# Performance work log

Measured on AMD Instinct MI355X. Metric: run time of the kernel, lower is better.

Reference implementation:

```python
import jax, jax.numpy as jnp
import numpy as np

B, S, H = 2, 2048, 2048
NH, NKV, HD = 16, 4, 128
GROUPS = NH // NKV
THETA = 10000.0
EPS = 1e-6


def setup_inputs() -> dict:
    key = jax.random.key(0)
    ks = jax.random.split(key, 6)
    scale = 0.02
    return {
        "hidden_states": jax.random.normal(ks[0], (B, S, H), jnp.float32),
        "wq": jax.random.normal(ks[1], (NH * HD, H), jnp.float32) * scale,
        "wk": jax.random.normal(ks[2], (NKV * HD, H), jnp.float32) * scale,
        "wv": jax.random.normal(ks[3], (NKV * HD, H), jnp.float32) * scale,
        "wo": jax.random.normal(ks[4], (H, NH * HD), jnp.float32) * scale,
        "q_norm_weight": jnp.ones((HD,), jnp.float32),
        "k_norm_weight": jnp.ones((HD,), jnp.float32),
    }


def _rope_tables(seq_len):
    inv_freq = 1.0 / (THETA ** (jnp.arange(0, HD, 2, dtype=jnp.float32) / HD))
    t = jnp.arange(seq_len, dtype=jnp.float32)
    freqs = jnp.outer(t, inv_freq)              # [S, HD/2]
    emb = jnp.concatenate([freqs, freqs], -1)   # [S, HD]
    return jnp.cos(emb), jnp.sin(emb)


def _rotate_half(x):
    x1, x2 = x[..., : HD // 2], x[..., HD // 2:]
    return jnp.concatenate([-x2, x1], -1)


def _rmsnorm(x, w):
    var = jnp.mean(jnp.square(x), axis=-1, keepdims=True)
    return x * jax.lax.rsqrt(var + EPS) * w


def reference(hidden_states, wq, wk, wv, wo, q_norm_weight, k_norm_weight):
    b, s, _ = hidden_states.shape
    q = (hidden_states @ wq.T).reshape(b, s, NH, HD).transpose(0, 2, 1, 3)    # [b,nh,s,d]
    k = (hidden_states @ wk.T).reshape(b, s, NKV, HD).transpose(0, 2, 1, 3)   # [b,nkv,s,d]
    v = (hidden_states @ wv.T).reshape(b, s, NKV, HD).transpose(0, 2, 1, 3)

    cos, sin = _rope_tables(s)                  # [s,d]
    q = q * cos + _rotate_half(q) * sin
    k = k * cos + _rotate_half(k) * sin

    # fused QK RMSNorm (applied inside fused_qknorm_flash_attention)
    q = _rmsnorm(q, q_norm_weight)
    k = _rmsnorm(k, k_norm_weight)

    # GQA: share each kv head across GROUPS query heads without materializing repeats
    qg = q.reshape(b, NKV, GROUPS, s, HD)
    scale = 1.0 / jnp.sqrt(jnp.float32(HD))
    scores = jnp.einsum('bhgqd,bhkd->bhgqk', qg, k) * scale   # [b,nkv,g,s,s]
    causal = jnp.tril(jnp.ones((s, s), bool))
    scores = jnp.where(causal, scores, jnp.finfo(scores.dtype).min)
    probs = jax.nn.softmax(scores, axis=-1)
    out = jnp.einsum('bhgqk,bhkd->bhgqd', probs, v)            # [b,nkv,g,s,d]
    out = out.reshape(b, NH, s, HD).transpose(0, 2, 1, 3).reshape(b, s, NH * HD)
    return out @ wo.T
```

## Files before the change

kernel.cpp:

```cpp
#include <hip/hip_runtime.h>
#include <math.h>

typedef __bf16 bf16;
typedef __bf16 bf16x8 __attribute__((ext_vector_type(8)));
typedef __bf16 bf16x4 __attribute__((ext_vector_type(4)));
typedef float f32x4 __attribute__((ext_vector_type(4)));

#define B_DIM 2
#define S_LEN 2048
#define H_DIM 2048
#define NH 16
#define NKV 4
#define HD 128

__device__ __forceinline__ void gl_lds16(const void* g, void* l) {
    __builtin_amdgcn_global_load_lds(
        (const __attribute__((address_space(1))) unsigned int*)g,
        (__attribute__((address_space(3))) unsigned int*)l, 16, 0, 0);
}

__global__ void cast_kernel(const float* __restrict__ src, bf16* __restrict__ dst, int n4) {
    int i = blockIdx.x * 256 + threadIdx.x;
    if (i >= n4) return;
    float4 f = ((const float4*)src)[i];
    bf16x4 o = { (bf16)f.x, (bf16)f.y, (bf16)f.z, (bf16)f.w };
    *(bf16x4*)(dst + (size_t)i * 4) = o;
}

template <typename OutT>
__global__ __launch_bounds__(256) void gemm_bt(const bf16* __restrict__ A,
                                               const bf16* __restrict__ Bt,
                                               OutT* __restrict__ C,
                                               int M, int N, int K) {
    __shared__ __align__(16) bf16 As[128 * 32];
    __shared__ __align__(16) bf16 Bs[128 * 32];
    const int t = threadIdx.x;
    const int lane = t & 63, w = t >> 6;
    const int wm = (w & 1) * 64, wn = (w >> 1) * 64;
    const int lr = lane & 15, quad = lane >> 4;
    const int m0 = blockIdx.x * 128, n0 = blockIdx.y * 128;
    const int lrow = lane >> 2, lk = (lane & 3) * 8;
    f32x4 acc[4][4];
#pragma unroll
    for (int i = 0; i < 4; i++)
#pragma unroll
        for (int j = 0; j < 4; j++) acc[i][j] = (f32x4){0.f, 0.f, 0.f, 0.f};

    for (int k0 = 0; k0 < K; k0 += 32) {
        __syncthreads();
#pragma unroll
        for (int i = 0; i < 2; i++) {
            const int r0 = i * 64 + w * 16;
            gl_lds16(A + (size_t)(m0 + r0 + lrow) * K + k0 + lk, &As[r0 * 32]);
            gl_lds16(Bt + (size_t)(n0 + r0 + lrow) * K + k0 + lk, &Bs[r0 * 32]);
        }
        __syncthreads();
        bf16x8 af[4], bfr[4];
#pragma unroll
        for (int i = 0; i < 4; i++) af[i] = *(const bf16x8*)&As[(wm + i * 16 + lr) * 32 + quad * 8];
#pragma unroll
        for (int j = 0; j < 4; j++) bfr[j] = *(const bf16x8*)&Bs[(wn + j * 16 + lr) * 32 + quad * 8];
#pragma unroll
        for (int i = 0; i < 4; i++)
#pragma unroll
            for (int j = 0; j < 4; j++)
                acc[i][j] = __builtin_amdgcn_mfma_f32_16x16x32_bf16(af[i], bfr[j], acc[i][j], 0, 0, 0);
    }
#pragma unroll
    for (int i = 0; i < 4; i++) {
        int m = m0 + wm + i * 16 + quad * 4;
#pragma unroll
        for (int j = 0; j < 4; j++) {
            int n = n0 + wn + j * 16 + lr;
#pragma unroll
            for (int r = 0; r < 4; r++)
                C[(size_t)(m + r) * N + n] = (OutT)acc[i][j][r];
        }
    }
}

__global__ __launch_bounds__(256) void rope_rms(const bf16* __restrict__ qkv,
                                                const float* __restrict__ qw,
                                                const float* __restrict__ kw,
                                                bf16* __restrict__ qb,
                                                bf16* __restrict__ kb,
                                                bf16* __restrict__ vt) {
    const int tok = blockIdx.x;
    const int b = tok >> 11, s = tok & (S_LEN - 1);
    const int lane = threadIdx.x & 63, w = threadIdx.x >> 6;
    const bf16* row = qkv + (size_t)tok * 3072;
    const float inv = expf(-(float)lane * (9.210340371976184f / 64.f));
    const float ang = (float)s * inv;
    float s_, c_;
    sincosf(ang, &s_, &c_);
    const float wq1 = qw[lane], wq2 = qw[lane + 64];
    const float wk1 = kw[lane], wk2 = kw[lane + 64];
    for (int u = w; u < 24; u += 4) {
        if (u < 16) {
            const float x1 = (float)row[u * 128 + lane], x2 = (float)row[u * 128 + 64 + lane];
            float y1 = x1 * c_ - x2 * s_;
            float y2 = x2 * c_ + x1 * s_;
            float ss = y1 * y1 + y2 * y2;
#pragma unroll
            for (int m = 1; m < 64; m <<= 1) ss += __shfl_xor(ss, m);
            const float r = rsqrtf(ss * (1.f / 128.f) + 1e-6f);
            size_t o = ((size_t)(b * NH + u) * S_LEN + s) * HD;
            qb[o + lane]      = (bf16)(y1 * r * wq1);
            qb[o + 64 + lane] = (bf16)(y2 * r * wq2);
        } else if (u < 20) {
            const int kh = u - 16;
            const float x1 = (float)row[2048 + kh * 128 + lane], x2 = (float)row[2048 + kh * 128 + 64 + lane];
            float y1 = x1 * c_ - x2 * s_;
            float y2 = x2 * c_ + x1 * s_;
            float ss = y1 * y1 + y2 * y2;
#pragma unroll
            for (int m = 1; m < 64; m <<= 1) ss += __shfl_xor(ss, m);
            const float r = rsqrtf(ss * (1.f / 128.f) + 1e-6f);
            size_t base = (size_t)(b * NKV + kh) * 16 * 16384;
            kb[base + (size_t)(lane >> 3) * 16384 + s * 8 + (lane & 7)]       = (bf16)(y1 * r * wk1);
            kb[base + (size_t)(8 + (lane >> 3)) * 16384 + s * 8 + (lane & 7)] = (bf16)(y2 * r * wk2);
        } else {
            const int vh = u - 20;
            const float x1 = (float)row[2560 + vh * 128 + lane], x2 = (float)row[2560 + vh * 128 + 64 + lane];
            size_t base = ((size_t)(b * NKV + vh) * 256 + (s >> 3)) * 1024 + (s & 7);
            vt[base + (size_t)lane * 8]        = (bf16)x1;
            vt[base + (size_t)(lane + 64) * 8] = (bf16)x2;
        }
    }
}

__global__ __launch_bounds__(128, 2) void flash(const bf16* __restrict__ qg,
                                                const bf16* __restrict__ kg,
                                                const bf16* __restrict__ vg,
                                                bf16* __restrict__ attn) {
    const int idx = blockIdx.x;
    const int qt = 31 - (idx >> 5);
    const int hb = idx & 31;
    const int h = hb & 15, b = hb >> 4;
    const int kvh = h >> 2;
    const bf16* qh = qg + (size_t)(b * NH + h) * S_LEN * HD;
    const bf16* kh = kg + (size_t)(b * NKV + kvh) * (16 * 16384);
    const bf16* vh = vg + (size_t)(b * NKV + kvh) * (256 * 1024);
    __shared__ __align__(16) bf16 Ks[16 * 512];
    __shared__ __align__(16) bf16 Vs[8 * 1152];
    __shared__ __align__(16) bf16 Ps[2][32 * 72];
    const int t = threadIdx.x, lane = t & 63, w = t >> 6, lr = lane & 15, quad = lane >> 4;
    bf16* psw = Ps[w];
    {
        const bf16 one = (bf16)1.0f;
        bf16x8 one8 = {one, one, one, one, one, one, one, one};
        *(bf16x8*)&Vs[(t >> 4) * 1152 + 1024 + (t & 15) * 8] = one8;
    }
    const int row0 = qt * 64 + w * 32;
    bf16x8 qf[2][4];
#pragma unroll
    for (int mg = 0; mg < 2; mg++)
#pragma unroll
        for (int c = 0; c < 4; c++)
            qf[mg][c] = *(const bf16x8*)(qh + (size_t)(row0 + mg * 16 + lr) * HD + c * 32 + quad * 8);
    f32x4 o[2][8];
    f32x4 lacc[2];
#pragma unroll
    for (int mg = 0; mg < 2; mg++) {
        lacc[mg] = (f32x4){0.f, 0.f, 0.f, 0.f};
#pragma unroll
        for (int j = 0; j < 8; j++) o[mg][j] = (f32x4){0.f, 0.f, 0.f, 0.f};
    }
    const float C1 = 0.12751744f;
    const float C2 = -17.3123405f;
    const int ntile = qt + 1;

    for (int kt = 0; kt < ntile; ++kt) {
        const int kbase = kt * 64;
        __syncthreads();
#pragma unroll
        for (int i = 0; i < 8; i++) {
            const int dc = w * 8 + i;
            gl_lds16(kh + (size_t)dc * 16384 + (size_t)kbase * 8 + lane * 8, &Ks[dc * 512]);
        }
#pragma unroll
        for (int i = 0; i < 4; i++) {
            const int c = w * 4 + i;
            const bf16* src = vh + ((size_t)(kbase >> 3) + c) * 1024 + lane * 8;
            gl_lds16(src, &Vs[c * 1152]);
            gl_lds16(src + 512, &Vs[c * 1152 + 512]);
        }
        __syncthreads();
        f32x4 sacc[2][4];
#pragma unroll
        for (int mg = 0; mg < 2; mg++)
#pragma unroll
            for (int n = 0; n < 4; n++) sacc[mg][n] = (f32x4){0.f, 0.f, 0.f, 0.f};
#pragma unroll
        for (int n = 0; n < 4; n++)
#pragma unroll
            for (int c = 0; c < 4; c++) {
                bf16x8 kf = *(const bf16x8*)&Ks[(c * 4 + quad) * 512 + (n * 16 + lr) * 8];
                sacc[0][n] = __builtin_amdgcn_mfma_f32_16x16x32_bf16(qf[0][c], kf, sacc[0][n], 0, 0, 0);
                sacc[1][n] = __builtin_amdgcn_mfma_f32_16x16x32_bf16(qf[1][c], kf, sacc[1][n], 0, 0, 0);
            }
        const bool diag = (kt == qt);
#pragma unroll
        for (int mg = 0; mg < 2; mg++)
#pragma unroll
            for (int n = 0; n < 4; n++)
#pragma unroll
                for (int r = 0; r < 4; r++) {
                    float e = exp2f(fmaf(sacc[mg][n][r], C1, C2));
                    if (diag) {
                        const int key = kbase + n * 16 + lr;
                        const int qrow = row0 + mg * 16 + quad * 4 + r;
                        e = (key <= qrow) ? e : 0.f;
                    }
                    psw[(mg * 16 + quad * 4 + r) * 72 + n * 16 + lr] = (bf16)e;
                }
        bf16x8 pf[2][2];
#pragma unroll
        for (int mg = 0; mg < 2; mg++)
#pragma unroll
            for (int k2 = 0; k2 < 2; k2++)
                pf[mg][k2] = *(const bf16x8*)&psw[(mg * 16 + lr) * 72 + k2 * 32 + quad * 8];
#pragma unroll
        for (int k2 = 0; k2 < 2; k2++) {
#pragma unroll
            for (int j = 0; j < 8; j++) {
                bf16x8 vf = *(const bf16x8*)&Vs[(k2 * 4 + quad) * 1152 + (j * 16 + lr) * 8];
                o[0][j] = __builtin_amdgcn_mfma_f32_16x16x32_bf16(pf[0][k2], vf, o[0][j], 0, 0, 0);
                o[1][j] = __builtin_amdgcn_mfma_f32_16x16x32_bf16(pf[1][k2], vf, o[1][j], 0, 0, 0);
            }
            bf16x8 vone = *(const bf16x8*)&Vs[(k2 * 4 + quad) * 1152 + (128 + lr) * 8];
            lacc[0] = __builtin_amdgcn_mfma_f32_16x16x32_bf16(pf[0][k2], vone, lacc[0], 0, 0, 0);
            lacc[1] = __builtin_amdgcn_mfma_f32_16x16x32_bf16(pf[1][k2], vone, lacc[1], 0, 0, 0);
        }
    }
#pragma unroll
    for (int mg = 0; mg < 2; mg++) {
        float inv[4];
#pragma unroll
        for (int r = 0; r < 4; r++) inv[r] = 1.0f / lacc[mg][r];
#pragma unroll
        for (int j = 0; j < 8; j++)
#pragma unroll
            for (int r = 0; r < 4; r++) {
                const int qrow = row0 + mg * 16 + quad * 4 + r;
                attn[((size_t)(b * S_LEN) + qrow) * (NH * HD) + h * HD + j * 16 + lr] =
                    (bf16)(o[mg][j][r] * inv[r]);
            }
    }
}

extern "C" void kernel_launch(void* const* d_in, const int* in_sizes, int n_in,
                              void* d_out, int out_size, void* d_ws, size_t ws_size,
                              hipStream_t stream) {
    (void)in_sizes; (void)n_in; (void)out_size; (void)ws_size;
    const float* hs  = (const float*)d_in[0];
    const float* wq  = (const float*)d_in[1];
    const float* wk  = (const float*)d_in[2];
    const float* wv  = (const float*)d_in[3];
    const float* wo  = (const float*)d_in[4];
    const float* qnw = (const float*)d_in[5];
    const float* knw = (const float*)d_in[6];
    float* out = (float*)d_out;

    char* ws = (char*)d_ws;
    size_t off = 0;
    auto alloc = [&](size_t bytes) {
        void* p = ws + off;
        off += (bytes + 255) & ~(size_t)255;
        return p;
    };
    bf16* hs_bf   = (bf16*)alloc((size_t)4096 * 2048 * 2);
    bf16* wqkv_bf = (bf16*)alloc((size_t)3072 * 2048 * 2);
    bf16* wo_bf   = (bf16*)alloc((size_t)2048 * 2048 * 2);
    bf16* qkv_bf  = (bf16*)alloc((size_t)4096 * 3072 * 2);
    bf16* q_bf    = (bf16*)alloc((size_t)B_DIM * NH * S_LEN * HD * 2);
    bf16* k_bf    = (bf16*)alloc((size_t)B_DIM * NKV * S_LEN * HD * 2);
    bf16* vt_bf   = (bf16*)alloc((size_t)B_DIM * NKV * S_LEN * HD * 2);
    bf16* at_bf   = (bf16*)alloc((size_t)4096 * 2048 * 2);

    cast_kernel<<<8192, 256, 0, stream>>>(hs, hs_bf, 2097152);
    cast_kernel<<<4096, 256, 0, stream>>>(wq, wqkv_bf, 1048576);
    cast_kernel<<<1024, 256, 0, stream>>>(wk, wqkv_bf + 4194304, 262144);
    cast_kernel<<<1024, 256, 0, stream>>>(wv, wqkv_bf + 5242880, 262144);
    cast_kernel<<<4096, 256, 0, stream>>>(wo, wo_bf, 1048576);

    gemm_bt<bf16><<<dim3(32, 24), 256, 0, stream>>>(hs_bf, wqkv_bf, qkv_bf, 4096, 3072, 2048);
    rope_rms<<<4096, 256, 0, stream>>>(qkv_bf, qnw, knw, q_bf, k_bf, vt_bf);
    flash<<<dim3(1024), 128, 0, stream>>>(q_bf, k_bf, vt_bf, at_bf);
    gemm_bt<float><<<dim3(32, 16), 256, 0, stream>>>(at_bf, wo_bf, out, 4096, 2048, 2048);
}
```

Measured before the change: 352.3 us.

## Enlarge flash query tile to 128 rows and fuse weight casts into one kernel

```diff
diff --git a/kernel.cpp b/kernel.cpp
--- a/kernel.cpp
+++ b/kernel.cpp
@@ -19,10 +19,21 @@
         (__attribute__((address_space(3))) unsigned int*)l, 16, 0, 0);
 }
 
-__global__ void cast_kernel(const float* __restrict__ src, bf16* __restrict__ dst, int n4) {
-    int i = blockIdx.x * 256 + threadIdx.x;
-    if (i >= n4) return;
-    float4 f = ((const float4*)src)[i];
+__global__ __launch_bounds__(256) void cast_all(const float* __restrict__ s0,
+                                                const float* __restrict__ s1,
+                                                const float* __restrict__ s2,
+                                                const float* __restrict__ s3,
+                                                const float* __restrict__ s4,
+                                                bf16* __restrict__ dst) {
+    const int i = blockIdx.x * 256 + threadIdx.x;
+    const float* src;
+    int off;
+    if (i < 2097152)      { src = s0; off = 0; }
+    else if (i < 3145728) { src = s1; off = 2097152; }
+    else if (i < 3407872) { src = s2; off = 3145728; }
+    else if (i < 3670016) { src = s3; off = 3407872; }
+    else                  { src = s4; off = 3670016; }
+    float4 f = ((const float4*)src)[i - off];
     bf16x4 o = { (bf16)f.x, (bf16)f.y, (bf16)f.z, (bf16)f.w };
     *(bf16x4*)(dst + (size_t)i * 4) = o;
 }
@@ -129,12 +140,12 @@
     }
 }
 
-__global__ __launch_bounds__(128, 2) void flash(const bf16* __restrict__ qg,
+__global__ __launch_bounds__(256, 2) void flash(const bf16* __restrict__ qg,
                                                 const bf16* __restrict__ kg,
                                                 const bf16* __restrict__ vg,
                                                 bf16* __restrict__ attn) {
     const int idx = blockIdx.x;
-    const int qt = 31 - (idx >> 5);
+    const int qt = 15 - (idx >> 5);
     const int hb = idx & 31;
     const int h = hb & 15, b = hb >> 4;
     const int kvh = h >> 2;
@@ -143,15 +154,15 @@
     const bf16* vh = vg + (size_t)(b * NKV + kvh) * (256 * 1024);
     __shared__ __align__(16) bf16 Ks[16 * 512];
     __shared__ __align__(16) bf16 Vs[8 * 1152];
-    __shared__ __align__(16) bf16 Ps[2][32 * 72];
+    __shared__ __align__(16) bf16 Ps[4][32 * 72];
     const int t = threadIdx.x, lane = t & 63, w = t >> 6, lr = lane & 15, quad = lane >> 4;
     bf16* psw = Ps[w];
-    {
+    if (t < 128) {
         const bf16 one = (bf16)1.0f;
         bf16x8 one8 = {one, one, one, one, one, one, one, one};
         *(bf16x8*)&Vs[(t >> 4) * 1152 + 1024 + (t & 15) * 8] = one8;
     }
-    const int row0 = qt * 64 + w * 32;
+    const int row0 = qt * 128 + w * 32;
     bf16x8 qf[2][4];
 #pragma unroll
     for (int mg = 0; mg < 2; mg++)
@@ -168,19 +179,19 @@
     }
     const float C1 = 0.12751744f;
     const float C2 = -17.3123405f;
-    const int ntile = qt + 1;
+    const int ntile = 2 * qt + 2;
 
     for (int kt = 0; kt < ntile; ++kt) {
         const int kbase = kt * 64;
         __syncthreads();
 #pragma unroll
-        for (int i = 0; i < 8; i++) {
-            const int dc = w * 8 + i;
+        for (int i = 0; i < 4; i++) {
+            const int dc = w * 4 + i;
             gl_lds16(kh + (size_t)dc * 16384 + (size_t)kbase * 8 + lane * 8, &Ks[dc * 512]);
         }
 #pragma unroll
-        for (int i = 0; i < 4; i++) {
-            const int c = w * 4 + i;
+        for (int i = 0; i < 2; i++) {
+            const int c = w * 2 + i;
             const bf16* src = vh + ((size_t)(kbase >> 3) + c) * 1024 + lane * 8;
             gl_lds16(src, &Vs[c * 1152]);
             gl_lds16(src + 512, &Vs[c * 1152 + 512]);
@@ -199,7 +210,7 @@
                 sacc[0][n] = __builtin_amdgcn_mfma_f32_16x16x32_bf16(qf[0][c], kf, sacc[0][n], 0, 0, 0);
                 sacc[1][n] = __builtin_amdgcn_mfma_f32_16x16x32_bf16(qf[1][c], kf, sacc[1][n], 0, 0, 0);
             }
-        const bool diag = (kt == qt);
+        const bool diag = (kt >= 2 * qt);
 #pragma unroll
         for (int mg = 0; mg < 2; mg++)
 #pragma unroll
@@ -278,14 +289,9 @@
     bf16* vt_bf   = (bf16*)alloc((size_t)B_DIM * NKV * S_LEN * HD * 2);
     bf16* at_bf   = (bf16*)alloc((size_t)4096 * 2048 * 2);
 
-    cast_kernel<<<8192, 256, 0, stream>>>(hs, hs_bf, 2097152);
-    cast_kernel<<<4096, 256, 0, stream>>>(wq, wqkv_bf, 1048576);
-    cast_kernel<<<1024, 256, 0, stream>>>(wk, wqkv_bf + 4194304, 262144);
-    cast_kernel<<<1024, 256, 0, stream>>>(wv, wqkv_bf + 5242880, 262144);
-    cast_kernel<<<4096, 256, 0, stream>>>(wo, wo_bf, 1048576);
-
+    cast_all<<<18432, 256, 0, stream>>>(hs, wq, wk, wv, wo, hs_bf);
     gemm_bt<bf16><<<dim3(32, 24), 256, 0, stream>>>(hs_bf, wqkv_bf, qkv_bf, 4096, 3072, 2048);
     rope_rms<<<4096, 256, 0, stream>>>(qkv_bf, qnw, knw, q_bf, k_bf, vt_bf);
-    flash<<<dim3(1024), 128, 0, stream>>>(q_bf, k_bf, vt_bf, at_bf);
+    flash<<<dim3(512), 256, 0, stream>>>(q_bf, k_bf, vt_bf, at_bf);
     gemm_bt<float><<<dim3(32, 16), 256, 0, stream>>>(at_bf, wo_bf, out, 4096, 2048, 2048);
 }
```

New measurement: 337.9 us. 1.04x faster.
